# Kernel optimization log

Measured on AMD Instinct MI355X. Metric: run time of the kernel, lower is better.

## Reference

```python
import jax, jax.numpy as jnp
import numpy as np

IMG = 640
TOPK = 13
NC = 1
ALPHA = 0.5
BETA = 6.0
EPS = 1e-9
IOU_EPS = 1e-7


def _make_anchors():
    pts = []
    for s in (8, 16, 32):
        n = IMG // s
        g = (jnp.arange(n, dtype=jnp.float32) + 0.5) * s
        yy, xx = jnp.meshgrid(g, g, indexing="ij")
        pts.append(jnp.stack([xx.ravel(), yy.ravel()], axis=-1))
    return jnp.concatenate(pts, axis=0)  # [8400, 2]


def _make_boxes(key, prefix):
    k1, k2 = jax.random.split(key)
    cxcy = jax.random.uniform(k1, prefix + (2,), minval=32.0, maxval=IMG - 32.0)
    wh = jax.random.uniform(k2, prefix + (2,), minval=8.0, maxval=128.0)
    return jnp.concatenate([cxcy - wh / 2, cxcy + wh / 2], axis=-1)


def setup_inputs() -> dict:
    key = jax.random.key(0)
    B, G, NA = 32, 64, 8400
    k1, k2, k3, k4 = jax.random.split(key, 4)
    pd_scores = jax.random.uniform(k1, (B, NA, 1))
    pd_bboxes = _make_boxes(k2, (B, NA))
    anc_points = _make_anchors()
    gt_labels = jnp.zeros((B, G, 1), dtype=jnp.int64)  # single class
    gt_bboxes = _make_boxes(k3, (B, G))
    num_gt = jax.random.randint(k4, (B, 1), 1, G + 1)
    mask_gt = (jnp.arange(G)[None, :] < num_gt).astype(jnp.float32)[..., None]
    return {
        "pd_scores": pd_scores,
        "pd_bboxes": pd_bboxes,
        "anc_points": anc_points,
        "gt_labels": gt_labels,
        "gt_bboxes": gt_bboxes,
        "mask_gt": mask_gt,
    }


def _iou_xyxy(gt, pd):
    # gt: [B,G,1,4], pd: [B,1,NA,4] -> [B,G,NA]
    ix1 = jnp.maximum(gt[..., 0], pd[..., 0])
    iy1 = jnp.maximum(gt[..., 1], pd[..., 1])
    ix2 = jnp.minimum(gt[..., 2], pd[..., 2])
    iy2 = jnp.minimum(gt[..., 3], pd[..., 3])
    inter = jnp.clip(ix2 - ix1, 0) * jnp.clip(iy2 - iy1, 0)
    a1 = (gt[..., 2] - gt[..., 0]) * (gt[..., 3] - gt[..., 1])
    a2 = (pd[..., 2] - pd[..., 0]) * (pd[..., 3] - pd[..., 1])
    return inter / (a1 + a2 - inter + IOU_EPS)


def reference(pd_scores, pd_bboxes, anc_points, gt_labels, gt_bboxes, mask_gt):
    B, G, _ = gt_bboxes.shape
    NA = pd_bboxes.shape[1]

    # candidates inside GT boxes: [B,G,NA]
    ap = anc_points[None, None]                   # [1,1,NA,2]
    gb = gt_bboxes[:, :, None]                    # [B,G,1,4]
    lt = ap - gb[..., :2]
    rb = gb[..., 2:] - ap
    mask_in_gts = (jnp.concatenate([lt, rb], axis=-1).min(axis=-1) > 0).astype(jnp.float32)
    valid_mask = mask_in_gts * mask_gt[..., 0][:, :, None]

    # pairwise IoU + alignment metric
    overlaps = jnp.clip(_iou_xyxy(gt_bboxes[:, :, None], pd_bboxes[:, None]), 0)  # [B,G,NA]
    bbox_scores = pd_scores[..., 0][:, None, :]                                   # [B,1,NA]
    align_metric = jnp.clip(bbox_scores, 0) ** ALPHA * overlaps ** BETA * valid_mask

    # top-k per GT over anchors (threshold-based mask, including ties, like torch ref)
    k = min(TOPK, NA)
    topk_vals = jax.lax.top_k(align_metric, k)[0]          # [B,G,k]
    threshold = topk_vals[..., -1:]
    mask_topk = (align_metric >= threshold).astype(jnp.float32)

    mask_pos = mask_topk * valid_mask

    # conflict resolution: anchor claimed by >1 GT -> GT with max IoU
    fg = mask_pos.sum(axis=1)                              # [B,NA]
    disputed = fg[:, None, :] > 1                          # [B,1,NA]
    best_gt = jnp.argmax(overlaps, axis=1)                 # [B,NA]
    one_hot_gt = (jnp.arange(G)[None, :, None] == best_gt[:, None, :]).astype(jnp.float32)
    mask_pos = jnp.where(disputed, one_hot_gt, mask_pos)
    fg_mask = mask_pos.sum(axis=1)                         # [B,NA]
    target_gt_idx = jnp.argmax(mask_pos, axis=1)           # [B,NA]

    # gather targets
    target_labels = jnp.clip(
        jnp.take_along_axis(gt_labels[..., 0], target_gt_idx, axis=1), 0)      # [B,NA]
    target_bboxes = jnp.take_along_axis(gt_bboxes, target_gt_idx[..., None], axis=1)  # [B,NA,4]
    target_scores = jax.nn.one_hot(target_labels, NC, dtype=jnp.float32) * fg_mask[..., None]

    # alignment normalization
    am = align_metric * mask_pos
    pos_align_max = am.max(axis=-1, keepdims=True)
    pos_iou_max = (overlaps * mask_pos).max(axis=-1, keepdims=True)
    norm_weights = (am / (pos_align_max + EPS) * pos_iou_max).max(axis=1)       # [B,NA]
    target_scores = target_scores * norm_weights[..., None]

    return target_labels, target_bboxes, target_scores, fg_mask > 0
```

## Files before the change

kernel.cpp:

```cpp
#include <hip/hip_runtime.h>

#define TOPK_K 13
#define KPAD 16
#define PCAP 384


__device__ __forceinline__ float iou_clip(const float4 g, const float4 p) {
    float ix1 = fmaxf(g.x, p.x), iy1 = fmaxf(g.y, p.y);
    float ix2 = fminf(g.z, p.z), iy2 = fminf(g.w, p.w);
    float iw = fmaxf(ix2 - ix1, 0.f);
    float ih = fmaxf(iy2 - iy1, 0.f);
    float inter = iw * ih;
    float a1 = (g.z - g.x) * (g.w - g.y);
    float a2 = (p.z - p.x) * (p.w - p.y);
    float iou = inter / (a1 + a2 - inter + 1e-7f);
    return fmaxf(iou, 0.f);
}

__device__ __forceinline__ float in_box(float ax, float ay, const float4 g) {
    float m = fminf(fminf(ax - g.x, ay - g.y), fminf(g.z - ax, g.w - ay));
    return (m > 0.f) ? 1.f : 0.f;
}

__device__ __forceinline__ float align_metric_f(float sqs, float iou, float valid) {
    float p2 = iou * iou;
    float p6 = p2 * p2 * p2;
    return sqs * p6 * valid;
}

__global__ __launch_bounds__(256) void k_thresh(
    const float* __restrict__ pd_scores, const float* __restrict__ pd_bboxes,
    const float* __restrict__ gt_bboxes, const float* __restrict__ mask_gt,
    float* __restrict__ thr, int* __restrict__ pam, int* __restrict__ pim,
    int B, int G, int NA)
{
    __shared__ float plist[4][PCAP];
    __shared__ int   pcnt[4];

    int w4 = threadIdx.x >> 6;
    int lane = threadIdx.x & 63;
    int w = blockIdx.x * 4 + w4;
    bool wok = (w < B * G);
    bool valid = wok && (mask_gt[w] != 0.f);

    if (lane == 0) pcnt[w4] = 0;
    __syncthreads();

    if (valid) {
        int b = w / G;
        float4 gb = *(const float4*)(gt_bboxes + (size_t)w * 4);
        const float* ps = pd_scores + (size_t)b * NA;
        const float* pb = pd_bboxes + (size_t)b * NA * 4;

        #pragma unroll
        for (int lvl = 0; lvl < 3; ++lvl) {
            const int n   = (lvl == 0) ? 80 : (lvl == 1 ? 40 : 20);
            const int off = (lvl == 0) ? 0  : (lvl == 1 ? 6400 : 8000);
            const float sf = (float)(8 << lvl);
            int ix0 = max(0,     (int)floorf(gb.x / sf - 0.5f));
            int iy0 = max(0,     (int)floorf(gb.y / sf - 0.5f));
            int ix1 = min(n - 1, (int)ceilf (gb.z / sf - 0.5f));
            int iy1 = min(n - 1, (int)ceilf (gb.w / sf - 0.5f));
            int wdt = ix1 - ix0 + 1, hgt = iy1 - iy0 + 1;
            if (wdt <= 0 || hgt <= 0) continue;
            int n_c = wdt * hgt;
            for (int c = lane; c < n_c; c += 64) {
                int ix = ix0 + (c % wdt);
                int iy = iy0 + (c / wdt);
                float ax = (ix + 0.5f) * sf;
                float ay = (iy + 0.5f) * sf;
                if (in_box(ax, ay, gb) != 0.f) {
                    int a = off + iy * n + ix;
                    float4 p = *(const float4*)(pb + (size_t)a * 4);
                    float iou = iou_clip(gb, p);
                    float sqs = sqrtf(fmaxf(ps[a], 0.f));
                    float am = align_metric_f(sqs, iou, 1.f);
                    if (am > 0.f) {
                        int idx = atomicAdd(&pcnt[w4], 1);
                        if (idx < PCAP) plist[w4][idx] = am;
                    }
                }
            }
        }
    }
    __syncthreads();

    float thrv = 0.f;
    if (valid && pcnt[w4] >= TOPK_K) {
        int n = pcnt[w4];
        float t[KPAD];
        #pragma unroll
        for (int i = 0; i < KPAD; ++i) t[i] = 0.f;
        for (int j = lane; j < n; j += 64) {
            float v = plist[w4][j];
            if (v > t[KPAD - 1]) {
                t[KPAD - 1] = v;
                #pragma unroll
                for (int i = KPAD - 1; i > 0; --i) {
                    float hi = fmaxf(t[i - 1], t[i]);
                    float lo = fminf(t[i - 1], t[i]);
                    t[i - 1] = hi; t[i] = lo;
                }
            }
        }
        for (int off = 1; off < 64; off <<= 1) {
            float o[KPAD], m[KPAD];
            #pragma unroll
            for (int i = 0; i < KPAD; ++i) o[i] = __shfl_xor(t[i], off, 64);
            #pragma unroll
            for (int i = 0; i < KPAD; ++i) m[i] = fmaxf(t[i], o[KPAD - 1 - i]);
            #pragma unroll
            for (int s = 8; s >= 1; s >>= 1) {
                #pragma unroll
                for (int i = 0; i < KPAD; ++i) {
                    if ((i & s) == 0) {
                        float hi = fmaxf(m[i], m[i + s]);
                        float lo = fminf(m[i], m[i + s]);
                        m[i] = hi; m[i + s] = lo;
                    }
                }
            }
            #pragma unroll
            for (int i = 0; i < KPAD; ++i) t[i] = m[i];
        }
        thrv = t[TOPK_K - 1];
    }

    if (wok && lane == 0) {
        thr[w] = thrv;
        pam[w] = 0;
        pim[w] = 0;
    }
}

__global__ __launch_bounds__(256) void k_assign(
    const float* __restrict__ pd_scores, const float* __restrict__ pd_bboxes,
    const float* __restrict__ anc, const int* __restrict__ gt_labels,
    const float* __restrict__ gt_bboxes, const float* __restrict__ mask_gt,
    const float* __restrict__ thr,
    float* __restrict__ out_labels, float* __restrict__ out_bboxes,
    float* __restrict__ out_fg,
    int* __restrict__ ws_tgt, float* __restrict__ ws_amv,
    int* __restrict__ pam, int* __restrict__ pim,
    int B, int G, int NA)
{
    __shared__ float4 sbox[64];
    __shared__ float  smask[64];
    __shared__ float  sthr[64];
    __shared__ int    slab[64];

    int b = blockIdx.y;
    int tid = threadIdx.x;
    if (tid < 64) {
        sbox[tid]  = *(const float4*)(gt_bboxes + ((size_t)b * G + tid) * 4);
        smask[tid] = mask_gt[b * G + tid];
        sthr[tid]  = thr[b * G + tid];
        int l = gt_labels[b * G + tid];
        slab[tid]  = (l < 0) ? 0 : l;
    }
    __syncthreads();

    int a = blockIdx.x * blockDim.x + tid;
    bool act = (a < NA);
    int lane = tid & 63;
    int ac = act ? a : (NA - 1);
    size_t o = (size_t)b * NA + ac;

    float4 p = *(const float4*)(pd_bboxes + o * 4);
    float ax = anc[2 * ac], ay = anc[2 * ac + 1];
    float sqs = sqrtf(fmaxf(pd_scores[o], 0.f));

    int fg = 0, firstg = 0;
    for (int g = 0; g < 64; ++g) {
        float4 gbb = sbox[g];
        bool cand = act && (in_box(ax, ay, gbb) != 0.f) && (smask[g] != 0.f);
        if (__any(cand)) {
            float iou = iou_clip(gbb, p);
            float am = align_metric_f(sqs, iou, 1.f);
            bool pass = cand && (am >= sthr[g]);
            if (pass) { if (fg == 0) firstg = g; ++fg; }
        }
    }

    int tgt = (fg == 1) ? firstg : 0;

    float4 gl = sbox[lane];
    unsigned long long dm = __ballot(fg > 1);
    while (dm) {
        int l = __ffsll((long long)dm) - 1;
        dm &= dm - 1;
        float4 pl;
        pl.x = __shfl(p.x, l, 64); pl.y = __shfl(p.y, l, 64);
        pl.z = __shfl(p.z, l, 64); pl.w = __shfl(p.w, l, 64);
        float iou = iou_clip(gl, pl);
        int g = lane;
        #pragma unroll
        for (int off = 32; off >= 1; off >>= 1) {
            float oi = __shfl_xor(iou, off, 64);
            int   og = __shfl_xor(g,   off, 64);
            if (oi > iou || (oi == iou && og < g)) { iou = oi; g = og; }
        }
        if (lane == l) tgt = g;
    }

    if (!act) return;

    float4 gbt = sbox[tgt];
    float vt  = in_box(ax, ay, gbt) * smask[tgt];
    float iout = iou_clip(gbt, p);
    float amt = align_metric_f(sqs, iout, vt);
    bool isfg = (fg != 0);
    float amv = isfg ? amt : 0.f;
    float iov = isfg ? iout : 0.f;

    out_labels[o] = (float)slab[tgt];
    *(float4*)(out_bboxes + o * 4) = gbt;
    out_fg[o] = isfg ? 1.f : 0.f;
    ws_tgt[o] = tgt;
    ws_amv[o] = amv;

    if (isfg) {
        int gi = b * G + tgt;
        atomicMax(&pam[gi], __float_as_int(amv));
        atomicMax(&pim[gi], __float_as_int(iov));
    }
}

__global__ __launch_bounds__(256) void k_scores(
    const int* __restrict__ ws_tgt, const float* __restrict__ ws_amv,
    const int* __restrict__ pam, const int* __restrict__ pim,
    const float* __restrict__ out_labels,
    float* __restrict__ out_scores,
    int B, int G, int NA)
{
    __shared__ int spam[64];
    __shared__ int spim[64];

    int b = blockIdx.y;
    int tid = threadIdx.x;
    if (tid < 64) {
        spam[tid] = pam[b * G + tid];
        spim[tid] = pim[b * G + tid];
    }
    __syncthreads();

    int a = blockIdx.x * blockDim.x + tid;
    if (a >= NA) return;
    size_t o = (size_t)b * NA + a;

    int tgt = ws_tgt[o];
    float amv = ws_amv[o];
    float pa = __int_as_float(spam[tgt]);
    float pi = __int_as_float(spim[tgt]);
    float wgt = amv / (pa + 1e-9f) * pi;
    float onehot = (out_labels[o] == 0.f) ? 1.f : 0.f;
    out_scores[o] = onehot * wgt;
}

extern "C" void kernel_launch(void* const* d_in, const int* in_sizes, int n_in,
                              void* d_out, int out_size, void* d_ws, size_t ws_size,
                              hipStream_t stream) {
    const float* pd_scores = (const float*)d_in[0];
    const float* pd_bboxes = (const float*)d_in[1];
    const float* anc       = (const float*)d_in[2];
    const int*   gt_labels = (const int*)d_in[3];
    const float* gt_bboxes = (const float*)d_in[4];
    const float* mask_gt   = (const float*)d_in[5];

    int NA = in_sizes[2] / 2;
    int B  = in_sizes[0] / NA;
    int G  = in_sizes[4] / (B * 4);

    float* out = (float*)d_out;
    float* out_labels = out;
    float* out_bboxes = out_labels + (size_t)B * NA;
    float* out_scores = out_bboxes + (size_t)B * NA * 4;
    float* out_fg     = out_scores + (size_t)B * NA;

    int BG = B * G;
    int BNA = B * NA;
    float* thr    = (float*)d_ws;
    int*   pam    = (int*)(thr + BG);
    int*   pim    = pam + BG;
    int*   ws_tgt = pim + BG;
    float* ws_amv = (float*)(ws_tgt + BNA);

    k_thresh<<<dim3((BG + 3) / 4), dim3(256), 0, stream>>>(
        pd_scores, pd_bboxes, gt_bboxes, mask_gt, thr, pam, pim, B, G, NA);

    k_assign<<<dim3((NA + 255) / 256, B), dim3(256), 0, stream>>>(
        pd_scores, pd_bboxes, anc, gt_labels, gt_bboxes, mask_gt, thr,
        out_labels, out_bboxes, out_fg, ws_tgt, ws_amv, pam, pim, B, G, NA);

    k_scores<<<dim3((NA + 255) / 256, B), dim3(256), 0, stream>>>(
        ws_tgt, ws_amv, pam, pim, out_labels, out_scores, B, G, NA);
}
```

Measured before the change: 47.27 us.

## Precompute per-anchor GT claim bitmasks in GT kernel, drop per-anchor GT loop

The per-GT kernel now marks, with 64-bit atomic OR, every in-box anchor it covers. After computing its top-k threshold it clears, with atomic AND, the bits of anchors whose alignment metric falls below that threshold. The assign kernel then reads one 64-bit mask per anchor and derives the foreground count and target GT with popcount and find-first-set. This replaces the 64-iteration GT scan with IoU recomputation in the assign kernel. In exchange it adds a memset of a B*NA 64-bit workspace, a second scan over each GT's candidate anchors, and global atomics.

```diff
diff --git a/kernel.cpp b/kernel.cpp
--- a/kernel.cpp
+++ b/kernel.cpp
@@ -28,10 +28,10 @@
     return sqs * p6 * valid;
 }
 
-__global__ __launch_bounds__(256) void k_thresh(
+__global__ __launch_bounds__(256) void k_gt(
     const float* __restrict__ pd_scores, const float* __restrict__ pd_bboxes,
     const float* __restrict__ gt_bboxes, const float* __restrict__ mask_gt,
-    float* __restrict__ thr, int* __restrict__ pam, int* __restrict__ pim,
+    unsigned long long* __restrict__ claim,
     int B, int G, int NA)
 {
     __shared__ float plist[4][PCAP];
@@ -40,96 +40,120 @@
     int w4 = threadIdx.x >> 6;
     int lane = threadIdx.x & 63;
     int w = blockIdx.x * 4 + w4;
-    bool wok = (w < B * G);
-    bool valid = wok && (mask_gt[w] != 0.f);
+    if (w >= B * G) return;
+    if (mask_gt[w] == 0.f) return;
+
+    int b = w / G;
+    int g = w - b * G;
+    float4 gb = *(const float4*)(gt_bboxes + (size_t)w * 4);
+    const float* ps = pd_scores + (size_t)b * NA;
+    const float* pb = pd_bboxes + (size_t)b * NA * 4;
+    unsigned long long* clb = claim + (size_t)b * NA;
+    const unsigned long long gbit = 1ull << g;
 
     if (lane == 0) pcnt[w4] = 0;
-    __syncthreads();
-
-    if (valid) {
-        int b = w / G;
-        float4 gb = *(const float4*)(gt_bboxes + (size_t)w * 4);
-        const float* ps = pd_scores + (size_t)b * NA;
-        const float* pb = pd_bboxes + (size_t)b * NA * 4;
-
-        #pragma unroll
-        for (int lvl = 0; lvl < 3; ++lvl) {
-            const int n   = (lvl == 0) ? 80 : (lvl == 1 ? 40 : 20);
-            const int off = (lvl == 0) ? 0  : (lvl == 1 ? 6400 : 8000);
-            const float sf = (float)(8 << lvl);
-            int ix0 = max(0,     (int)floorf(gb.x / sf - 0.5f));
-            int iy0 = max(0,     (int)floorf(gb.y / sf - 0.5f));
-            int ix1 = min(n - 1, (int)ceilf (gb.z / sf - 0.5f));
-            int iy1 = min(n - 1, (int)ceilf (gb.w / sf - 0.5f));
-            int wdt = ix1 - ix0 + 1, hgt = iy1 - iy0 + 1;
-            if (wdt <= 0 || hgt <= 0) continue;
-            int n_c = wdt * hgt;
-            for (int c = lane; c < n_c; c += 64) {
-                int ix = ix0 + (c % wdt);
-                int iy = iy0 + (c / wdt);
-                float ax = (ix + 0.5f) * sf;
-                float ay = (iy + 0.5f) * sf;
-                if (in_box(ax, ay, gb) != 0.f) {
-                    int a = off + iy * n + ix;
-                    float4 p = *(const float4*)(pb + (size_t)a * 4);
-                    float iou = iou_clip(gb, p);
-                    float sqs = sqrtf(fmaxf(ps[a], 0.f));
-                    float am = align_metric_f(sqs, iou, 1.f);
-                    if (am > 0.f) {
-                        int idx = atomicAdd(&pcnt[w4], 1);
-                        if (idx < PCAP) plist[w4][idx] = am;
-                    }
+
+    int rix0[3], riy0[3], rix1[3], riy1[3];
+    #pragma unroll
+    for (int lvl = 0; lvl < 3; ++lvl) {
+        const int n = (lvl == 0) ? 80 : (lvl == 1 ? 40 : 20);
+        const float sf = (float)(8 << lvl);
+        rix0[lvl] = max(0,     (int)floorf(gb.x / sf - 0.5f));
+        riy0[lvl] = max(0,     (int)floorf(gb.y / sf - 0.5f));
+        rix1[lvl] = min(n - 1, (int)ceilf (gb.z / sf - 0.5f));
+        riy1[lvl] = min(n - 1, (int)ceilf (gb.w / sf - 0.5f));
+    }
+
+    #pragma unroll
+    for (int lvl = 0; lvl < 3; ++lvl) {
+        const int n   = (lvl == 0) ? 80 : (lvl == 1 ? 40 : 20);
+        const int off = (lvl == 0) ? 0  : (lvl == 1 ? 6400 : 8000);
+        const float sf = (float)(8 << lvl);
+        int wdt = rix1[lvl] - rix0[lvl] + 1, hgt = riy1[lvl] - riy0[lvl] + 1;
+        if (wdt <= 0 || hgt <= 0) continue;
+        int n_c = wdt * hgt;
+        for (int c = lane; c < n_c; c += 64) {
+            int ix = rix0[lvl] + (c % wdt);
+            int iy = riy0[lvl] + (c / wdt);
+            float ax = (ix + 0.5f) * sf;
+            float ay = (iy + 0.5f) * sf;
+            if (in_box(ax, ay, gb) != 0.f) {
+                int a = off + iy * n + ix;
+                atomicOr(&clb[a], gbit);
+                float4 p = *(const float4*)(pb + (size_t)a * 4);
+                float iou = iou_clip(gb, p);
+                float sqs = sqrtf(fmaxf(ps[a], 0.f));
+                float am = align_metric_f(sqs, iou, 1.f);
+                if (am > 0.f) {
+                    int idx = atomicAdd(&pcnt[w4], 1);
+                    if (idx < PCAP) plist[w4][idx] = am;
                 }
             }
         }
     }
-    __syncthreads();
-
-    float thrv = 0.f;
-    if (valid && pcnt[w4] >= TOPK_K) {
-        int n = pcnt[w4];
-        float t[KPAD];
-        #pragma unroll
-        for (int i = 0; i < KPAD; ++i) t[i] = 0.f;
-        for (int j = lane; j < n; j += 64) {
-            float v = plist[w4][j];
-            if (v > t[KPAD - 1]) {
-                t[KPAD - 1] = v;
-                #pragma unroll
-                for (int i = KPAD - 1; i > 0; --i) {
-                    float hi = fmaxf(t[i - 1], t[i]);
-                    float lo = fminf(t[i - 1], t[i]);
-                    t[i - 1] = hi; t[i] = lo;
+
+    if (pcnt[w4] < TOPK_K) return;
+
+    int n = pcnt[w4];
+    float t[KPAD];
+    #pragma unroll
+    for (int i = 0; i < KPAD; ++i) t[i] = 0.f;
+    for (int j = lane; j < n; j += 64) {
+        float v = plist[w4][j];
+        if (v > t[KPAD - 1]) {
+            t[KPAD - 1] = v;
+            #pragma unroll
+            for (int i = KPAD - 1; i > 0; --i) {
+                float hi = fmaxf(t[i - 1], t[i]);
+                float lo = fminf(t[i - 1], t[i]);
+                t[i - 1] = hi; t[i] = lo;
+            }
+        }
+    }
+    for (int off = 1; off < 64; off <<= 1) {
+        float o[KPAD], m[KPAD];
+        #pragma unroll
+        for (int i = 0; i < KPAD; ++i) o[i] = __shfl_xor(t[i], off, 64);
+        #pragma unroll
+        for (int i = 0; i < KPAD; ++i) m[i] = fmaxf(t[i], o[KPAD - 1 - i]);
+        #pragma unroll
+        for (int s = 8; s >= 1; s >>= 1) {
+            #pragma unroll
+            for (int i = 0; i < KPAD; ++i) {
+                if ((i & s) == 0) {
+                    float hi = fmaxf(m[i], m[i + s]);
+                    float lo = fminf(m[i], m[i + s]);
+                    m[i] = hi; m[i + s] = lo;
                 }
             }
         }
-        for (int off = 1; off < 64; off <<= 1) {
-            float o[KPAD], m[KPAD];
-            #pragma unroll
-            for (int i = 0; i < KPAD; ++i) o[i] = __shfl_xor(t[i], off, 64);
-            #pragma unroll
-            for (int i = 0; i < KPAD; ++i) m[i] = fmaxf(t[i], o[KPAD - 1 - i]);
-            #pragma unroll
-            for (int s = 8; s >= 1; s >>= 1) {
-                #pragma unroll
-                for (int i = 0; i < KPAD; ++i) {
-                    if ((i & s) == 0) {
-                        float hi = fmaxf(m[i], m[i + s]);
-                        float lo = fminf(m[i], m[i + s]);
-                        m[i] = hi; m[i + s] = lo;
-                    }
-                }
+        #pragma unroll
+        for (int i = 0; i < KPAD; ++i) t[i] = m[i];
+    }
+    float thr = t[TOPK_K - 1];
+
+    #pragma unroll
+    for (int lvl = 0; lvl < 3; ++lvl) {
+        const int n2  = (lvl == 0) ? 80 : (lvl == 1 ? 40 : 20);
+        const int off = (lvl == 0) ? 0  : (lvl == 1 ? 6400 : 8000);
+        const float sf = (float)(8 << lvl);
+        int wdt = rix1[lvl] - rix0[lvl] + 1, hgt = riy1[lvl] - riy0[lvl] + 1;
+        if (wdt <= 0 || hgt <= 0) continue;
+        int n_c = wdt * hgt;
+        for (int c = lane; c < n_c; c += 64) {
+            int ix = rix0[lvl] + (c % wdt);
+            int iy = riy0[lvl] + (c / wdt);
+            float ax = (ix + 0.5f) * sf;
+            float ay = (iy + 0.5f) * sf;
+            if (in_box(ax, ay, gb) != 0.f) {
+                int a = off + iy * n2 + ix;
+                float4 p = *(const float4*)(pb + (size_t)a * 4);
+                float iou = iou_clip(gb, p);
+                float sqs = sqrtf(fmaxf(ps[a], 0.f));
+                float am = align_metric_f(sqs, iou, 1.f);
+                if (am < thr) atomicAnd(&clb[a], ~gbit);
             }
-            #pragma unroll
-            for (int i = 0; i < KPAD; ++i) t[i] = m[i];
-        }
-        thrv = t[TOPK_K - 1];
-    }
-
-    if (wok && lane == 0) {
-        thr[w] = thrv;
-        pam[w] = 0;
-        pim[w] = 0;
+        }
     }
 }
 
@@ -137,7 +161,7 @@
     const float* __restrict__ pd_scores, const float* __restrict__ pd_bboxes,
     const float* __restrict__ anc, const int* __restrict__ gt_labels,
     const float* __restrict__ gt_bboxes, const float* __restrict__ mask_gt,
-    const float* __restrict__ thr,
+    const unsigned long long* __restrict__ claim,
     float* __restrict__ out_labels, float* __restrict__ out_bboxes,
     float* __restrict__ out_fg,
     int* __restrict__ ws_tgt, float* __restrict__ ws_amv,
@@ -146,7 +170,6 @@
 {
     __shared__ float4 sbox[64];
     __shared__ float  smask[64];
-    __shared__ float  sthr[64];
     __shared__ int    slab[64];
 
     int b = blockIdx.y;
@@ -154,7 +177,6 @@
     if (tid < 64) {
         sbox[tid]  = *(const float4*)(gt_bboxes + ((size_t)b * G + tid) * 4);
         smask[tid] = mask_gt[b * G + tid];
-        sthr[tid]  = thr[b * G + tid];
         int l = gt_labels[b * G + tid];
         slab[tid]  = (l < 0) ? 0 : l;
     }
@@ -166,23 +188,11 @@
     int ac = act ? a : (NA - 1);
     size_t o = (size_t)b * NA + ac;
 
+    unsigned long long cw = act ? claim[o] : 0ull;
     float4 p = *(const float4*)(pd_bboxes + o * 4);
-    float ax = anc[2 * ac], ay = anc[2 * ac + 1];
-    float sqs = sqrtf(fmaxf(pd_scores[o], 0.f));
-
-    int fg = 0, firstg = 0;
-    for (int g = 0; g < 64; ++g) {
-        float4 gbb = sbox[g];
-        bool cand = act && (in_box(ax, ay, gbb) != 0.f) && (smask[g] != 0.f);
-        if (__any(cand)) {
-            float iou = iou_clip(gbb, p);
-            float am = align_metric_f(sqs, iou, 1.f);
-            bool pass = cand && (am >= sthr[g]);
-            if (pass) { if (fg == 0) firstg = g; ++fg; }
-        }
-    }
-
-    int tgt = (fg == 1) ? firstg : 0;
+
+    int fg = (int)__popcll(cw);
+    int tgt = (fg == 1) ? (__ffsll((long long)cw) - 1) : 0;
 
     float4 gl = sbox[lane];
     unsigned long long dm = __ballot(fg > 1);
@@ -206,6 +216,8 @@
     if (!act) return;
 
     float4 gbt = sbox[tgt];
+    float ax = anc[2 * ac], ay = anc[2 * ac + 1];
+    float sqs = sqrtf(fmaxf(pd_scores[o], 0.f));
     float vt  = in_box(ax, ay, gbt) * smask[tgt];
     float iout = iou_clip(gbt, p);
     float amt = align_metric_f(sqs, iout, vt);
@@ -279,17 +291,19 @@
 
     int BG = B * G;
     int BNA = B * NA;
-    float* thr    = (float*)d_ws;
-    int*   pam    = (int*)(thr + BG);
+    unsigned long long* claim = (unsigned long long*)d_ws;
+    int*   pam    = (int*)(claim + BNA);
     int*   pim    = pam + BG;
     int*   ws_tgt = pim + BG;
     float* ws_amv = (float*)(ws_tgt + BNA);
 
-    k_thresh<<<dim3((BG + 3) / 4), dim3(256), 0, stream>>>(
-        pd_scores, pd_bboxes, gt_bboxes, mask_gt, thr, pam, pim, B, G, NA);
+    hipMemsetAsync(claim, 0, (size_t)BNA * 8 + (size_t)BG * 8, stream);
+
+    k_gt<<<dim3((BG + 3) / 4), dim3(256), 0, stream>>>(
+        pd_scores, pd_bboxes, gt_bboxes, mask_gt, claim, B, G, NA);
 
     k_assign<<<dim3((NA + 255) / 256, B), dim3(256), 0, stream>>>(
-        pd_scores, pd_bboxes, anc, gt_labels, gt_bboxes, mask_gt, thr,
+        pd_scores, pd_bboxes, anc, gt_labels, gt_bboxes, mask_gt, claim,
         out_labels, out_bboxes, out_fg, ws_tgt, ws_amv, pam, pim, B, G, NA);
 
     k_scores<<<dim3((NA + 255) / 256, B), dim3(256), 0, stream>>>(
```

After: 47.11 us. Within noise of the previous version (-0.3%).

## Cull GT boxes per anchor block and widen threshold kernel to a block per GT

Applied to the files above, without the earlier changes.

The threshold kernel now assigns a full 256-thread block to each GT box instead of one wavefront per box, spreading candidate scanning over more threads. The assign kernel computes anchor coordinates analytically instead of loading them. It also builds a per-block list of GT boxes whose extents overlap the block's anchor bounding box, so each thread loops only over relevant GTs. This removes wasted in-box checks and the loads from the anchor array, at the cost of an extra reduction and barrier and a launch with four times as many threshold blocks.

```diff
diff --git a/kernel.cpp b/kernel.cpp
--- a/kernel.cpp
+++ b/kernel.cpp
@@ -28,71 +28,80 @@
     return sqs * p6 * valid;
 }
 
+__device__ __forceinline__ void anc_xy(int i, float& ax, float& ay) {
+    int lvl = (i < 6400) ? 0 : (i < 8000 ? 1 : 2);
+    int n   = (lvl == 0) ? 80 : (lvl == 1 ? 40 : 20);
+    int off = (lvl == 0) ? 0  : (lvl == 1 ? 6400 : 8000);
+    float sf = (float)(8 << lvl);
+    int r = i - off;
+    int iy = r / n, ix = r - iy * n;
+    ax = (ix + 0.5f) * sf;
+    ay = (iy + 0.5f) * sf;
+}
+
 __global__ __launch_bounds__(256) void k_thresh(
     const float* __restrict__ pd_scores, const float* __restrict__ pd_bboxes,
     const float* __restrict__ gt_bboxes, const float* __restrict__ mask_gt,
     float* __restrict__ thr, int* __restrict__ pam, int* __restrict__ pim,
     int B, int G, int NA)
 {
-    __shared__ float plist[4][PCAP];
-    __shared__ int   pcnt[4];
-
-    int w4 = threadIdx.x >> 6;
-    int lane = threadIdx.x & 63;
-    int w = blockIdx.x * 4 + w4;
-    bool wok = (w < B * G);
-    bool valid = wok && (mask_gt[w] != 0.f);
-
-    if (lane == 0) pcnt[w4] = 0;
-    __syncthreads();
-
-    if (valid) {
-        int b = w / G;
-        float4 gb = *(const float4*)(gt_bboxes + (size_t)w * 4);
-        const float* ps = pd_scores + (size_t)b * NA;
-        const float* pb = pd_bboxes + (size_t)b * NA * 4;
-
-        #pragma unroll
-        for (int lvl = 0; lvl < 3; ++lvl) {
-            const int n   = (lvl == 0) ? 80 : (lvl == 1 ? 40 : 20);
-            const int off = (lvl == 0) ? 0  : (lvl == 1 ? 6400 : 8000);
-            const float sf = (float)(8 << lvl);
-            int ix0 = max(0,     (int)floorf(gb.x / sf - 0.5f));
-            int iy0 = max(0,     (int)floorf(gb.y / sf - 0.5f));
-            int ix1 = min(n - 1, (int)ceilf (gb.z / sf - 0.5f));
-            int iy1 = min(n - 1, (int)ceilf (gb.w / sf - 0.5f));
-            int wdt = ix1 - ix0 + 1, hgt = iy1 - iy0 + 1;
-            if (wdt <= 0 || hgt <= 0) continue;
-            int n_c = wdt * hgt;
-            for (int c = lane; c < n_c; c += 64) {
-                int ix = ix0 + (c % wdt);
-                int iy = iy0 + (c / wdt);
-                float ax = (ix + 0.5f) * sf;
-                float ay = (iy + 0.5f) * sf;
-                if (in_box(ax, ay, gb) != 0.f) {
-                    int a = off + iy * n + ix;
-                    float4 p = *(const float4*)(pb + (size_t)a * 4);
-                    float iou = iou_clip(gb, p);
-                    float sqs = sqrtf(fmaxf(ps[a], 0.f));
-                    float am = align_metric_f(sqs, iou, 1.f);
-                    if (am > 0.f) {
-                        int idx = atomicAdd(&pcnt[w4], 1);
-                        if (idx < PCAP) plist[w4][idx] = am;
-                    }
+    __shared__ float plist[PCAP];
+    __shared__ int   pcnt;
+
+    int w = blockIdx.x;
+    int tid = threadIdx.x;
+    if (tid == 0) { pam[w] = 0; pim[w] = 0; pcnt = 0; }
+    __syncthreads();
+
+    if (mask_gt[w] == 0.f) { if (tid == 0) thr[w] = 0.f; return; }
+
+    int b = w / G;
+    float4 gb = *(const float4*)(gt_bboxes + (size_t)w * 4);
+    const float* ps = pd_scores + (size_t)b * NA;
+    const float* pb = pd_bboxes + (size_t)b * NA * 4;
+
+    #pragma unroll
+    for (int lvl = 0; lvl < 3; ++lvl) {
+        const int n   = (lvl == 0) ? 80 : (lvl == 1 ? 40 : 20);
+        const int off = (lvl == 0) ? 0  : (lvl == 1 ? 6400 : 8000);
+        const float sf = (float)(8 << lvl);
+        int ix0 = max(0,     (int)floorf(gb.x / sf - 0.5f));
+        int iy0 = max(0,     (int)floorf(gb.y / sf - 0.5f));
+        int ix1 = min(n - 1, (int)ceilf (gb.z / sf - 0.5f));
+        int iy1 = min(n - 1, (int)ceilf (gb.w / sf - 0.5f));
+        int wdt = ix1 - ix0 + 1, hgt = iy1 - iy0 + 1;
+        if (wdt <= 0 || hgt <= 0) continue;
+        int n_c = wdt * hgt;
+        for (int c = tid; c < n_c; c += 256) {
+            int ix = ix0 + (c % wdt);
+            int iy = iy0 + (c / wdt);
+            float ax = (ix + 0.5f) * sf;
+            float ay = (iy + 0.5f) * sf;
+            if (in_box(ax, ay, gb) != 0.f) {
+                int a = off + iy * n + ix;
+                float4 p = *(const float4*)(pb + (size_t)a * 4);
+                float iou = iou_clip(gb, p);
+                float sqs = sqrtf(fmaxf(ps[a], 0.f));
+                float am = align_metric_f(sqs, iou, 1.f);
+                if (am > 0.f) {
+                    int idx = atomicAdd(&pcnt, 1);
+                    if (idx < PCAP) plist[idx] = am;
                 }
             }
         }
     }
     __syncthreads();
 
-    float thrv = 0.f;
-    if (valid && pcnt[w4] >= TOPK_K) {
-        int n = pcnt[w4];
+    int n = pcnt;
+    if (n < TOPK_K) { if (tid == 0) thr[w] = 0.f; return; }
+
+    if (tid < 64) {
+        int lane = tid;
         float t[KPAD];
         #pragma unroll
         for (int i = 0; i < KPAD; ++i) t[i] = 0.f;
         for (int j = lane; j < n; j += 64) {
-            float v = plist[w4][j];
+            float v = plist[j];
             if (v > t[KPAD - 1]) {
                 t[KPAD - 1] = v;
                 #pragma unroll
@@ -123,19 +132,13 @@
             #pragma unroll
             for (int i = 0; i < KPAD; ++i) t[i] = m[i];
         }
-        thrv = t[TOPK_K - 1];
-    }
-
-    if (wok && lane == 0) {
-        thr[w] = thrv;
-        pam[w] = 0;
-        pim[w] = 0;
+        if (lane == 0) thr[w] = t[TOPK_K - 1];
     }
 }
 
 __global__ __launch_bounds__(256) void k_assign(
     const float* __restrict__ pd_scores, const float* __restrict__ pd_bboxes,
-    const float* __restrict__ anc, const int* __restrict__ gt_labels,
+    const int* __restrict__ gt_labels,
     const float* __restrict__ gt_bboxes, const float* __restrict__ mask_gt,
     const float* __restrict__ thr,
     float* __restrict__ out_labels, float* __restrict__ out_bboxes,
@@ -148,6 +151,9 @@
     __shared__ float  smask[64];
     __shared__ float  sthr[64];
     __shared__ int    slab[64];
+    __shared__ float  sred[4][4];
+    __shared__ int    slist[64];
+    __shared__ int    scount;
 
     int b = blockIdx.y;
     int tid = threadIdx.x;
@@ -158,27 +164,54 @@
         int l = gt_labels[b * G + tid];
         slab[tid]  = (l < 0) ? 0 : l;
     }
-    __syncthreads();
 
     int a = blockIdx.x * blockDim.x + tid;
     bool act = (a < NA);
     int lane = tid & 63;
+    int wv = tid >> 6;
     int ac = act ? a : (NA - 1);
     size_t o = (size_t)b * NA + ac;
 
+    float ax, ay; anc_xy(ac, ax, ay);
+
+    float mnx = ax, mxx = ax, mny = ay, mxy = ay;
+    #pragma unroll
+    for (int off = 32; off >= 1; off >>= 1) {
+        mnx = fminf(mnx, __shfl_xor(mnx, off, 64));
+        mxx = fmaxf(mxx, __shfl_xor(mxx, off, 64));
+        mny = fminf(mny, __shfl_xor(mny, off, 64));
+        mxy = fmaxf(mxy, __shfl_xor(mxy, off, 64));
+    }
+    if (lane == 0) { sred[wv][0] = mnx; sred[wv][1] = mxx; sred[wv][2] = mny; sred[wv][3] = mxy; }
+    __syncthreads();
+    float bmnx = fminf(fminf(sred[0][0], sred[1][0]), fminf(sred[2][0], sred[3][0]));
+    float bmxx = fmaxf(fmaxf(sred[0][1], sred[1][1]), fmaxf(sred[2][1], sred[3][1]));
+    float bmny = fminf(fminf(sred[0][2], sred[1][2]), fminf(sred[2][2], sred[3][2]));
+    float bmxy = fmaxf(fmaxf(sred[0][3], sred[1][3]), fmaxf(sred[2][3], sred[3][3]));
+
+    if (tid < 64) {
+        float4 gbb = sbox[tid];
+        bool el = (smask[tid] != 0.f) &&
+                  (gbb.x < bmxx) && (gbb.z > bmnx) &&
+                  (gbb.y < bmxy) && (gbb.w > bmny);
+        unsigned long long bal = __ballot(el);
+        if (el) slist[(int)__popcll(bal & ((1ull << tid) - 1ull))] = tid;
+        if (tid == 0) scount = (int)__popcll(bal);
+    }
+    __syncthreads();
+    int nsl = scount;
+
     float4 p = *(const float4*)(pd_bboxes + o * 4);
-    float ax = anc[2 * ac], ay = anc[2 * ac + 1];
     float sqs = sqrtf(fmaxf(pd_scores[o], 0.f));
 
     int fg = 0, firstg = 0;
-    for (int g = 0; g < 64; ++g) {
+    for (int j = 0; j < nsl; ++j) {
+        int g = slist[j];
         float4 gbb = sbox[g];
-        bool cand = act && (in_box(ax, ay, gbb) != 0.f) && (smask[g] != 0.f);
-        if (__any(cand)) {
+        if (act && in_box(ax, ay, gbb) != 0.f) {
             float iou = iou_clip(gbb, p);
             float am = align_metric_f(sqs, iou, 1.f);
-            bool pass = cand && (am >= sthr[g]);
-            if (pass) { if (fg == 0) firstg = g; ++fg; }
+            if (am >= sthr[g]) { if (fg == 0) firstg = g; ++fg; }
         }
     }
 
@@ -262,7 +295,6 @@
                               hipStream_t stream) {
     const float* pd_scores = (const float*)d_in[0];
     const float* pd_bboxes = (const float*)d_in[1];
-    const float* anc       = (const float*)d_in[2];
     const int*   gt_labels = (const int*)d_in[3];
     const float* gt_bboxes = (const float*)d_in[4];
     const float* mask_gt   = (const float*)d_in[5];
@@ -285,11 +317,11 @@
     int*   ws_tgt = pim + BG;
     float* ws_amv = (float*)(ws_tgt + BNA);
 
-    k_thresh<<<dim3((BG + 3) / 4), dim3(256), 0, stream>>>(
+    k_thresh<<<dim3(BG), dim3(256), 0, stream>>>(
         pd_scores, pd_bboxes, gt_bboxes, mask_gt, thr, pam, pim, B, G, NA);
 
     k_assign<<<dim3((NA + 255) / 256, B), dim3(256), 0, stream>>>(
-        pd_scores, pd_bboxes, anc, gt_labels, gt_bboxes, mask_gt, thr,
+        pd_scores, pd_bboxes, gt_labels, gt_bboxes, mask_gt, thr,
         out_labels, out_bboxes, out_fg, ws_tgt, ws_amv, pam, pim, B, G, NA);
 
     k_scores<<<dim3((NA + 255) / 256, B), dim3(256), 0, stream>>>(
```

Result: faster. 40.87 us (-13.5%).
